# Performance work log

Measured on AMD Instinct MI355X. Metric: run time of the kernel, lower is better.

The kernel has to match this reference:

```python
import jax, jax.numpy as jnp
import numpy as np

B, N, C = 8, 8192, 256
H = 8            # num_heads
D = C // H       # head dim = 32
P = 64           # proj_size (Linformer rank)


def setup_inputs() -> dict:
    key = jax.random.key(0)
    ks = jax.random.split(key, 12)
    s = lambda fan_in: 1.0 / np.sqrt(fan_in)
    return {
        "x": jax.random.normal(ks[0], (B, N, C), jnp.float32),
        "Wqkvv": jax.random.normal(ks[1], (4 * C, C), jnp.float32) * s(C),
        "WE": jax.random.normal(ks[2], (P, N), jnp.float32) * s(N),
        "bE": jax.random.normal(ks[3], (P,), jnp.float32) * s(N),
        "WF": jax.random.normal(ks[4], (P, N), jnp.float32) * s(N),
        "bF": jax.random.normal(ks[5], (P,), jnp.float32) * s(N),
        "Wo1": jax.random.normal(ks[6], (C // 2, C), jnp.float32) * s(C),
        "bo1": jax.random.normal(ks[7], (C // 2,), jnp.float32) * s(C),
        "Wo2": jax.random.normal(ks[8], (C // 2, C), jnp.float32) * s(C),
        "bo2": jax.random.normal(ks[9], (C // 2,), jnp.float32) * s(C),
        "temp1": jnp.ones((H, 1, 1), jnp.float32),
        "temp2": jnp.ones((H, 1, 1), jnp.float32),
    }


def _l2norm(v, axis=-1, eps=1e-12):
    # matches torch F.normalize
    n = jnp.sqrt(jnp.sum(v * v, axis=axis, keepdims=True))
    return v / jnp.maximum(n, eps)


def reference(x, Wqkvv, WE, bE, WF, bF, Wo1, bo1, Wo2, bo2, temp1, temp2):
    b, n, c = x.shape
    # qkvv: [b,n,4c] -> [4,b,h,d,n]  (includes the .transpose(-2,-1) of each part)
    qkvv = jnp.einsum('bnc,fc->bnf', x, Wqkvv).reshape(b, n, 4, H, D)
    qkvv = qkvv.transpose(2, 0, 3, 4, 1)
    q, k, v_ca, v_sa = qkvv[0], qkvv[1], qkvv[2], qkvv[3]  # each [b,h,d,n]

    # Linformer-style low-rank projections along the token axis
    k_proj = jnp.einsum('bhdn,pn->bhdp', k, WE) + bE   # [b,h,d,p]
    v_proj = jnp.einsum('bhdn,pn->bhdp', v_sa, WF) + bF

    qn = _l2norm(q)
    kn = _l2norm(k)

    # --- channel attention branch (XCiT-style) ---
    attn_ca = jnp.einsum('bhdn,bhen->bhde', qn, kn) * temp1[None]  # [b,h,d,d]
    attn_ca = jax.nn.softmax(attn_ca, axis=-1)  # dropout: eval mode (identity)
    x_ca = jnp.einsum('bhde,bhen->bhdn', attn_ca, v_ca)
    x_ca = x_ca.transpose(0, 3, 1, 2).reshape(b, n, c)  # [b,n,c]

    # --- spatial attention branch (low-rank) ---
    attn_sa = jnp.einsum('bhdn,bhdp->bhnp', qn, k_proj) * temp2[None]  # [b,h,n,p]
    attn_sa = jax.nn.softmax(attn_sa, axis=-1)
    x_sa = jnp.einsum('bhnp,bhdp->bhnd', attn_sa, v_proj)  # [b,h,n,d]
    # faithful to original: permute(0,3,1,2).reshape(b,n,c)
    x_sa = x_sa.transpose(0, 3, 1, 2).reshape(b, n, c)

    x_sa = jnp.einsum('bnc,oc->bno', x_sa, Wo1) + bo1
    x_ca = jnp.einsum('bnc,oc->bno', x_ca, Wo2) + bo2
    return jnp.concatenate((x_sa, x_ca), axis=-1)
```

## Files before the change

kernel.cpp:

```cpp
#include <hip/hip_runtime.h>
#include <hip/hip_bf16.h>
#include <stdint.h>


typedef __attribute__((ext_vector_type(8))) __bf16 bf16x8;
typedef __attribute__((ext_vector_type(4))) __bf16 bf16x4;
typedef __attribute__((ext_vector_type(4))) float f32x4;

#define MFMA(a, b, c) __builtin_amdgcn_mfma_f32_16x16x32_bf16((a), (b), (c), 0, 0, 0)

__device__ __forceinline__ void gl2lds16(const __bf16* g, __bf16* l) {
  __builtin_amdgcn_global_load_lds(
      (const __attribute__((address_space(1))) void*)(const void*)g,
      (__attribute__((address_space(3))) void*)(void*)l, 16, 0, 0);
}

__device__ __forceinline__ int detect_f32(const unsigned int* __restrict__ xw) {
  int c = 0;
#pragma unroll
  for (int i = 0; i < 64; ++i) {
    const unsigned int u = xw[i];
    c += (((u >> 7) & 0xFF) >= 0xC0) ? 1 : 0;
    c += (((u >> 23) & 0xFF) >= 0xC0) ? 1 : 0;
  }
  return c > 8;
}

__global__ __launch_bounds__(256) void k_convert_x(const void* __restrict__ src,
                                                   __bf16* __restrict__ dst,
                                                   float* __restrict__ nsum) {
  if (blockIdx.x == 0) {
#pragma unroll
    for (int j = 0; j < 16; ++j) nsum[threadIdx.x + j * 256] = 0.f;
  }
  const int i = (blockIdx.x * 256 + threadIdx.x) * 8;
  if (detect_f32((const unsigned int*)src)) {
    const float* s = (const float*)src;
    bf16x8 v;
#pragma unroll
    for (int j = 0; j < 8; ++j) v[j] = (__bf16)s[i + j];
    *(bf16x8*)(dst + i) = v;
  } else {
    *(bf16x8*)(dst + i) = *(const bf16x8*)((const __bf16*)src + i);
  }
}

__global__ __launch_bounds__(256) void k_convert_w(
    const void* s0, const void* s1, const void* s2, const void* s3, const void* s4,
    const void* s5, const void* s6, const void* s7, const void* s8, const void* s9,
    const void* s10, __bf16* __restrict__ cw, const void* __restrict__ xsrc) {
  const int i = (blockIdx.x * 256 + threadIdx.x) * 8;
  if (i >= 1376656) return;
  const void* s;
  int base;
  if (i < 262144)        { s = s0;  base = 0; }
  else if (i < 786432)   { s = s1;  base = 262144; }
  else if (i < 786496)   { s = s2;  base = 786432; }
  else if (i < 1310784)  { s = s3;  base = 786496; }
  else if (i < 1310848)  { s = s4;  base = 1310784; }
  else if (i < 1343616)  { s = s5;  base = 1310848; }
  else if (i < 1343744)  { s = s6;  base = 1343616; }
  else if (i < 1376512)  { s = s7;  base = 1343744; }
  else if (i < 1376640)  { s = s8;  base = 1376512; }
  else if (i < 1376648)  { s = s9;  base = 1376640; }
  else                   { s = s10; base = 1376648; }
  const int li = i - base;
  if (detect_f32((const unsigned int*)xsrc)) {
    const float* sf = (const float*)s;
#pragma unroll
    for (int j = 0; j < 8; ++j) cw[i + j] = (__bf16)sf[li + j];
  } else {
    const __bf16* sb = (const __bf16*)s;
#pragma unroll
    for (int j = 0; j < 8; ++j) cw[i + j] = sb[li + j];
  }
}

__global__ __launch_bounds__(256) void k_qkvv(const __bf16* __restrict__ x,
                                              const __bf16* __restrict__ Wq,
                                              __bf16* __restrict__ qkvv,
                                              float* __restrict__ qsum,
                                              float* __restrict__ ksum) {
  __shared__ alignas(16) __bf16 As[128 * 32];
  __shared__ alignas(16) __bf16 Bs[128 * 32];
  const int t = threadIdx.x, lane = t & 63;
  const int wr = t >> 7, wc = (t >> 6) & 1;
  const int l15 = lane & 15, g = lane >> 4;
  const int f0 = blockIdx.y * 128;
  const int t0 = blockIdx.x * 128;
  f32x4 acc[4][4] = {};
  const int r = t >> 2;
  const int c8 = ((t & 3) ^ ((t >> 3) & 3)) * 8;
  const int cx = ((g ^ ((l15 >> 1) & 3)) * 8);
  for (int k0 = 0; k0 < 256; k0 += 32) {
#pragma unroll
    for (int i = 0; i < 2; ++i) {
      gl2lds16(Wq + (size_t)(f0 + i * 64 + r) * 256 + k0 + c8, As + i * 2048 + t * 8);
      gl2lds16(x + (size_t)(t0 + i * 64 + r) * 256 + k0 + c8, Bs + i * 2048 + t * 8);
    }
    __syncthreads();
    bf16x8 af[4], bfr[4];
#pragma unroll
    for (int i = 0; i < 4; ++i) {
      af[i] = *(const bf16x8*)(As + (wr * 64 + i * 16 + l15) * 32 + cx);
      bfr[i] = *(const bf16x8*)(Bs + (wc * 64 + i * 16 + l15) * 32 + cx);
    }
#pragma unroll
    for (int i = 0; i < 4; ++i)
#pragma unroll
      for (int j = 0; j < 4; ++j) acc[i][j] = MFMA(af[i], bfr[j], acc[i][j]);
    __syncthreads();
  }
  const int b = t0 >> 13;
#pragma unroll
  for (int i = 0; i < 4; ++i) {
#pragma unroll
    for (int j = 0; j < 4; ++j) {
      const int tok = t0 + wc * 64 + j * 16 + l15;
      const int n = tok & 8191;
#pragma unroll
      for (int rr = 0; rr < 4; ++rr) {
        const int f = f0 + wr * 64 + i * 16 + g * 4 + rr;
        qkvv[(size_t)(((f >> 8) * 8 + b) * 256 + (f & 255)) * 8192 + n] = (__bf16)acc[i][j][rr];
      }
    }
  }
  if (f0 < 512) {
    float* dst = (f0 >> 8) ? ksum : qsum;
#pragma unroll
    for (int i = 0; i < 4; ++i) {
#pragma unroll
      for (int rr = 0; rr < 4; ++rr) {
        float s = 0.f;
#pragma unroll
        for (int j = 0; j < 4; ++j) {
          const float v = acc[i][j][rr];
          s += v * v;
        }
#pragma unroll
        for (int off = 1; off < 16; off <<= 1) s += __shfl_xor(s, off, 16);
        if (l15 == 0) {
          const int f = f0 + wr * 64 + i * 16 + g * 4 + rr;
          atomicAdd(dst + b * 256 + (f & 255), s);
        }
      }
    }
  }
}

__global__ __launch_bounds__(256) void k_proj_part(const __bf16* __restrict__ qkvv,
                                                   const __bf16* __restrict__ WE,
                                                   const __bf16* __restrict__ WF,
                                                   float* __restrict__ pbuf) {
  __shared__ alignas(16) __bf16 As[128 * 32];
  __shared__ alignas(16) __bf16 Bs[64 * 32];
  const int t = threadIdx.x, lane = t & 63;
  const int wr = t >> 7, wc = (t >> 6) & 1;
  const int l15 = lane & 15, g = lane >> 4;
  const int kc = blockIdx.x, mt = blockIdx.y, pj = blockIdx.z;
  const __bf16* A = qkvv + (size_t)(pj ? 3 : 1) * 2048 * 8192;
  const __bf16* Bm = pj ? WF : WE;
  const int r0 = mt * 128;
  f32x4 acc[4][2] = {};
  const int r = t >> 2;
  const int c8 = ((t & 3) ^ ((t >> 3) & 3)) * 8;
  const int cx = ((g ^ ((l15 >> 1) & 3)) * 8);
  for (int k0 = kc * 512; k0 < kc * 512 + 512; k0 += 32) {
#pragma unroll
    for (int i = 0; i < 2; ++i)
      gl2lds16(A + (size_t)(r0 + i * 64 + r) * 8192 + k0 + c8, As + i * 2048 + t * 8);
    gl2lds16(Bm + (size_t)r * 8192 + k0 + c8, Bs + t * 8);
    __syncthreads();
    bf16x8 af[4], bfr[2];
#pragma unroll
    for (int i = 0; i < 4; ++i)
      af[i] = *(const bf16x8*)(As + (wr * 64 + i * 16 + l15) * 32 + cx);
#pragma unroll
    for (int j = 0; j < 2; ++j)
      bfr[j] = *(const bf16x8*)(Bs + (wc * 32 + j * 16 + l15) * 32 + cx);
#pragma unroll
    for (int i = 0; i < 4; ++i)
#pragma unroll
      for (int j = 0; j < 2; ++j) acc[i][j] = MFMA(af[i], bfr[j], acc[i][j]);
    __syncthreads();
  }
  float* dst = pbuf + (size_t)((pj * 16 + kc) * 2048 + r0) * 64;
#pragma unroll
  for (int i = 0; i < 4; ++i)
#pragma unroll
    for (int j = 0; j < 2; ++j)
#pragma unroll
      for (int rr = 0; rr < 4; ++rr)
        dst[(wr * 64 + i * 16 + g * 4 + rr) * 64 + wc * 32 + j * 16 + l15] = acc[i][j][rr];
}

__global__ __launch_bounds__(256) void k_proj_reduce(const float* __restrict__ pbuf,
                                                     const __bf16* __restrict__ bE,
                                                     const __bf16* __restrict__ bF,
                                                     const float* __restrict__ qsum,
                                                     const __bf16* __restrict__ t2,
                                                     __bf16* __restrict__ kprojT,
                                                     __bf16* __restrict__ vprojb) {
  const int idx = blockIdx.x * 256 + threadIdx.x;
  const int pj = idx >> 17, rp = idx & 131071, p = idx & 63;
  const int row = rp >> 6, bh = row >> 5, d = row & 31, h = bh & 7;
  float s = (float)((pj ? bF : bE)[p]);
  const float* src = pbuf + (size_t)pj * 16 * 131072 + rp;
#pragma unroll
  for (int k = 0; k < 16; ++k) s += src[(size_t)k * 131072];
  if (pj == 0) {
    const float qi = 1.0f / fmaxf(sqrtf(qsum[row]), 1e-12f);
    kprojT[bh * 2048 + p * 32 + d] = (__bf16)(s * qi * (float)t2[h]);
  } else {
    vprojb[bh * 2048 + d * 64 + p] = (__bf16)s;
  }
}

__global__ __launch_bounds__(256) void k_sca_part(const __bf16* __restrict__ qkvv,
                                                  float* __restrict__ spart) {
  const int bh = blockIdx.x, kc = blockIdx.y;
  const int t = threadIdx.x, lane = t & 63, w = t >> 6;
  const __bf16* qb = qkvv + (size_t)(bh * 32) * 8192;
  const __bf16* kb = qkvv + (size_t)(2048 + bh * 32) * 8192;
  f32x4 acc[2][2] = {};
  const int kbase = kc * 1024 + w * 256 + (lane >> 4) * 8;
#pragma unroll
  for (int ks = 0; ks < 256; ks += 32) {
    bf16x8 af[2], bfr[2];
#pragma unroll
    for (int i = 0; i < 2; ++i) {
      af[i] = *(const bf16x8*)(qb + (size_t)(i * 16 + (lane & 15)) * 8192 + kbase + ks);
      bfr[i] = *(const bf16x8*)(kb + (size_t)(i * 16 + (lane & 15)) * 8192 + kbase + ks);
    }
#pragma unroll
    for (int i = 0; i < 2; ++i)
#pragma unroll
      for (int j = 0; j < 2; ++j) acc[i][j] = MFMA(af[i], bfr[j], acc[i][j]);
  }
  float* dst = spart + (size_t)((bh * 8 + kc) * 4 + w) * 1024;
#pragma unroll
  for (int i = 0; i < 2; ++i)
#pragma unroll
    for (int j = 0; j < 2; ++j)
#pragma unroll
      for (int rr = 0; rr < 4; ++rr)
        dst[(i * 16 + (lane >> 4) * 4 + rr) * 32 + j * 16 + (lane & 15)] = acc[i][j][rr];
}

__global__ __launch_bounds__(256) void k_sca_softmax(const float* __restrict__ spart,
                                                     const float* __restrict__ qsum,
                                                     const float* __restrict__ ksum,
                                                     const __bf16* __restrict__ temp1,
                                                     __bf16* __restrict__ attnb) {
  const int bh = blockIdx.x;
  __shared__ float S[1024];
  const int t = threadIdx.x;
  const float tmp = (float)temp1[bh & 7];
  for (int idx = t; idx < 1024; idx += 256) {
    float s = 0.f;
    const float* src = spart + (size_t)bh * 32768 + idx;
#pragma unroll
    for (int k = 0; k < 32; ++k) s += src[k * 1024];
    const float qi = 1.0f / fmaxf(sqrtf(qsum[bh * 32 + (idx >> 5)]), 1e-12f);
    const float ki = 1.0f / fmaxf(sqrtf(ksum[bh * 32 + (idx & 31)]), 1e-12f);
    S[idx] = s * qi * ki * tmp;
  }
  __syncthreads();
  const int lane = t & 63, w = t >> 6;
#pragma unroll
  for (int rr = 0; rr < 4; ++rr) {
    const int row = rr * 8 + w * 2 + (lane >> 5);
    const int e = lane & 31;
    float v = S[row * 32 + e];
    float m = v;
#pragma unroll
    for (int off = 16; off; off >>= 1) m = fmaxf(m, __shfl_xor(m, off, 32));
    const float ex = __expf(v - m);
    float sm = ex;
#pragma unroll
    for (int off = 16; off; off >>= 1) sm += __shfl_xor(sm, off, 32);
    attnb[(size_t)bh * 1024 + row * 32 + e] = (__bf16)(ex / sm);
  }
}

__global__ __launch_bounds__(256) void k_casa(const __bf16* __restrict__ qkvv,
                                              const __bf16* __restrict__ attnb,
                                              const __bf16* __restrict__ kprojT,
                                              const __bf16* __restrict__ vprojb,
                                              __bf16* __restrict__ xca,
                                              __bf16* __restrict__ xsa) {
  __shared__ __bf16 P[4][16 * 72];
  const int t = threadIdx.x, lane = t & 63, w = t >> 6;
  const int l15 = lane & 15, g = lane >> 4;
  if (blockIdx.y < 64) {
    const int bh = blockIdx.y, b = bh >> 3, h = bh & 7;
    const __bf16* vb = qkvv + (size_t)(4096 + bh * 32) * 8192;
    bf16x8 aa[2];
#pragma unroll
    for (int mi = 0; mi < 2; ++mi)
      aa[mi] = *(const bf16x8*)(attnb + bh * 1024 + (mi * 16 + l15) * 32 + g * 8);
#pragma unroll
    for (int it = 0; it < 4; ++it) {
      const int n = blockIdx.x * 256 + it * 64 + w * 16 + l15;
      union { bf16x8 v; unsigned short u[8]; } bq;
#pragma unroll
      for (int j = 0; j < 8; ++j)
        bq.u[j] = *(const unsigned short*)(vb + (size_t)(g * 8 + j) * 8192 + n);
      f32x4 o[2] = {};
#pragma unroll
      for (int mi = 0; mi < 2; ++mi) o[mi] = MFMA(aa[mi], bq.v, o[mi]);
#pragma unroll
      for (int mi = 0; mi < 2; ++mi) {
        bf16x4 p4;
#pragma unroll
        for (int rr = 0; rr < 4; ++rr) p4[rr] = (__bf16)o[mi][rr];
        *(bf16x4*)(xca + (size_t)(b * 8192 + n) * 256 + h * 32 + mi * 16 + g * 4) = p4;
      }
    }
  } else {
    const int bh = blockIdx.y - 64;
    const __bf16* qb = qkvv + (size_t)(bh * 32) * 8192;
    bf16x8 ka[4], va[2][2];
#pragma unroll
    for (int tile = 0; tile < 4; ++tile)
      ka[tile] = *(const bf16x8*)(kprojT + bh * 2048 + (tile * 16 + l15) * 32 + g * 8);
#pragma unroll
    for (int mi = 0; mi < 2; ++mi)
#pragma unroll
      for (int kh = 0; kh < 2; ++kh)
        va[mi][kh] = *(const bf16x8*)(vprojb + bh * 2048 + (mi * 16 + l15) * 64 + kh * 32 + g * 8);
    __bf16* Pw = &P[w][0];
#pragma unroll
    for (int it = 0; it < 4; ++it) {
      const int n0 = blockIdx.x * 256 + it * 64 + w * 16;
      union { bf16x8 v; unsigned short u[8]; } bq;
#pragma unroll
      for (int j = 0; j < 8; ++j)
        bq.u[j] = *(const unsigned short*)(qb + (size_t)(g * 8 + j) * 8192 + n0 + l15);
      f32x4 st[4];
#pragma unroll
      for (int tile = 0; tile < 4; ++tile) {
        f32x4 z = {};
        st[tile] = MFMA(ka[tile], bq.v, z);
      }
      float m = st[0][0];
#pragma unroll
      for (int tile = 0; tile < 4; ++tile)
#pragma unroll
        for (int rr = 0; rr < 4; ++rr) m = fmaxf(m, st[tile][rr]);
      m = fmaxf(m, __shfl_xor(m, 16, 64));
      m = fmaxf(m, __shfl_xor(m, 32, 64));
      float sum = 0.f;
#pragma unroll
      for (int tile = 0; tile < 4; ++tile) {
        bf16x4 p4;
#pragma unroll
        for (int rr = 0; rr < 4; ++rr) {
          const float ex = __expf(st[tile][rr] - m);
          sum += ex;
          p4[rr] = (__bf16)ex;
        }
        *(bf16x4*)(Pw + l15 * 72 + tile * 16 + g * 4) = p4;
      }
      sum += __shfl_xor(sum, 16, 64);
      sum += __shfl_xor(sum, 32, 64);
      const float inv = 1.0f / sum;
      f32x4 o[2] = {};
#pragma unroll
      for (int kh = 0; kh < 2; ++kh) {
        const bf16x8 pf = *(const bf16x8*)(Pw + l15 * 72 + kh * 32 + g * 8);
#pragma unroll
        for (int mi = 0; mi < 2; ++mi) o[mi] = MFMA(va[mi][kh], pf, o[mi]);
      }
#pragma unroll
      for (int mi = 0; mi < 2; ++mi)
#pragma unroll
        for (int rr = 0; rr < 4; ++rr) {
          const int d = mi * 16 + g * 4 + rr;
          xsa[(size_t)(bh * 32 + d) * 8192 + n0 + l15] = (__bf16)(o[mi][rr] * inv);
        }
    }
  }
}

__global__ __launch_bounds__(256) void k_out(const __bf16* __restrict__ xsa,
                                             const __bf16* __restrict__ xca,
                                             const __bf16* __restrict__ Wo1,
                                             const __bf16* __restrict__ bo1,
                                             const __bf16* __restrict__ Wo2,
                                             const __bf16* __restrict__ bo2,
                                             void* __restrict__ outv,
                                             const void* __restrict__ xsrc) {
  __shared__ alignas(16) __bf16 As[128 * 32];
  __shared__ alignas(16) __bf16 Bs[128 * 32];
  const int t = threadIdx.x, lane = t & 63;
  const int wr = t >> 7, wc = (t >> 6) & 1;
  const int l15 = lane & 15, g = lane >> 4;
  const int nt = blockIdx.x, b = blockIdx.y, br = blockIdx.z;
  const int isf32 = detect_f32((const unsigned int*)xsrc);
  const __bf16* Wo = br ? Wo2 : Wo1;
  const __bf16* bo = br ? bo2 : bo1;
  f32x4 acc[4][4] = {};
  const int r = t >> 2;
  const int c8 = ((t & 3) ^ ((t >> 3) & 3)) * 8;
  const int cx = ((g ^ ((l15 >> 1) & 3)) * 8);
  for (int k0 = 0; k0 < 256; k0 += 32) {
#pragma unroll
    for (int i = 0; i < 2; ++i) {
      const int row = nt * 128 + i * 64 + r;
      const __bf16* ga;
      if (br == 0) {
        ga = xsa + (size_t)((b * 8 + ((row >> 5) & 7)) * 32 + (row >> 8)) * 8192 +
             (row & 31) * 256 + k0 + c8;
      } else {
        ga = xca + (size_t)(b * 8192 + row) * 256 + k0 + c8;
      }
      gl2lds16(ga, As + i * 2048 + t * 8);
      gl2lds16(Wo + (size_t)(i * 64 + r) * 256 + k0 + c8, Bs + i * 2048 + t * 8);
    }
    __syncthreads();
    bf16x8 af[4], bfr[4];
#pragma unroll
    for (int i = 0; i < 4; ++i) {
      af[i] = *(const bf16x8*)(As + (wr * 64 + i * 16 + l15) * 32 + cx);
      bfr[i] = *(const bf16x8*)(Bs + (wc * 64 + i * 16 + l15) * 32 + cx);
    }
#pragma unroll
    for (int i = 0; i < 4; ++i)
#pragma unroll
      for (int j = 0; j < 4; ++j) acc[i][j] = MFMA(af[i], bfr[j], acc[i][j]);
    __syncthreads();
  }
  float bias[4];
#pragma unroll
  for (int j = 0; j < 4; ++j) bias[j] = (float)bo[wc * 64 + j * 16 + l15];
#pragma unroll
  for (int i = 0; i < 4; ++i) {
#pragma unroll
    for (int j = 0; j < 4; ++j) {
      const int col = wc * 64 + j * 16 + l15;
#pragma unroll
      for (int rr = 0; rr < 4; ++rr) {
        const int row = nt * 128 + wr * 64 + i * 16 + g * 4 + rr;
        const float val = acc[i][j][rr] + bias[j];
        const size_t oi = (size_t)(b * 8192 + row) * 256 + br * 128 + col;
        if (isf32) ((float*)outv)[oi] = val;
        else ((__bf16*)outv)[oi] = (__bf16)val;
      }
    }
  }
}

extern "C" void kernel_launch(void* const* d_in, const int* in_sizes, int n_in,
                              void* d_out, int out_size, void* d_ws, size_t ws_size,
                              hipStream_t stream) {
  char* ws = (char*)d_ws;
  __bf16* qkvv   = (__bf16*)(ws);
  __bf16* cinx   = (__bf16*)(ws + 134217728ull);
  __bf16* xca    = (__bf16*)(ws + 134217728ull);
  float*  pbuf   = (float*)(ws + 167772160ull);
  float*  spart  = (float*)(ws + 184549376ull);
  __bf16* xsa    = (__bf16*)(ws + 167772160ull);
  __bf16* kprojT = (__bf16*)(ws + 201326592ull);
  __bf16* vprojb = (__bf16*)(ws + 201588736ull);
  float*  qsum   = (float*)(ws + 201850880ull);
  float*  ksum   = (float*)(ws + 201859072ull);
  __bf16* attnb  = (__bf16*)(ws + 201867264ull);
  __bf16* cw     = (__bf16*)(ws + 201998336ull);

  __bf16* cWq  = cw;
  __bf16* cWE  = cw + 262144;
  __bf16* cbE  = cw + 786432;
  __bf16* cWF  = cw + 786496;
  __bf16* cbF  = cw + 1310784;
  __bf16* cWo1 = cw + 1310848;
  __bf16* cbo1 = cw + 1343616;
  __bf16* cWo2 = cw + 1343744;
  __bf16* cbo2 = cw + 1376512;
  __bf16* ct1  = cw + 1376640;
  __bf16* ct2  = cw + 1376648;

  k_convert_x<<<8192, 256, 0, stream>>>(d_in[0], cinx, qsum);
  k_convert_w<<<673, 256, 0, stream>>>(d_in[1], d_in[2], d_in[3], d_in[4], d_in[5],
                                       d_in[6], d_in[7], d_in[8], d_in[9], d_in[10],
                                       d_in[11], cw, d_in[0]);
  k_qkvv<<<dim3(512, 8), 256, 0, stream>>>(cinx, cWq, qkvv, qsum, ksum);
  k_proj_part<<<dim3(16, 16, 2), 256, 0, stream>>>(qkvv, cWE, cWF, pbuf);
  k_proj_reduce<<<dim3(1024), 256, 0, stream>>>(pbuf, cbE, cbF, qsum, ct2, kprojT, vprojb);
  k_sca_part<<<dim3(64, 8), 256, 0, stream>>>(qkvv, spart);
  k_sca_softmax<<<dim3(64), 256, 0, stream>>>(spart, qsum, ksum, ct1, attnb);
  k_casa<<<dim3(32, 128), 256, 0, stream>>>(qkvv, attnb, kprojT, vprojb, xca, xsa);
  k_out<<<dim3(64, 8, 2), 256, 0, stream>>>(xsa, xca, cWo1, cbo1, cWo2, cbo2, d_out, d_in[0]);
}
```

Before: 330.0 us.

## Stage QKVV epilogue through LDS for coalesced stores; replace norm atomics with partial reduction

The QKVV GEMM epilogue now transposes each 16-row accumulator slice through a shared-memory tile so that every thread writes 16-byte contiguous runs along the token axis, replacing scattered 2-byte stores. The squared-norm sums for q and k are computed from the bf16-rounded values and written as per-block partials, and a new small kernel reduces them, so float atomics and the zeroing in the convert kernel are no longer needed. This adds LDS traffic, extra barriers and one more kernel launch. The norms now come from bf16-rounded values rather than the fp32 accumulators.

Result: faster. 311.5 us (-5.6%).

```diff
diff --git a/kernel.cpp b/kernel.cpp
--- a/kernel.cpp
+++ b/kernel.cpp
@@ -27,12 +27,7 @@
 }
 
 __global__ __launch_bounds__(256) void k_convert_x(const void* __restrict__ src,
-                                                   __bf16* __restrict__ dst,
-                                                   float* __restrict__ nsum) {
-  if (blockIdx.x == 0) {
-#pragma unroll
-    for (int j = 0; j < 16; ++j) nsum[threadIdx.x + j * 256] = 0.f;
-  }
+                                                   __bf16* __restrict__ dst) {
   const int i = (blockIdx.x * 256 + threadIdx.x) * 8;
   if (detect_f32((const unsigned int*)src)) {
     const float* s = (const float*)src;
@@ -79,10 +74,10 @@
 __global__ __launch_bounds__(256) void k_qkvv(const __bf16* __restrict__ x,
                                               const __bf16* __restrict__ Wq,
                                               __bf16* __restrict__ qkvv,
-                                              float* __restrict__ qsum,
-                                              float* __restrict__ ksum) {
+                                              float* __restrict__ npart) {
   __shared__ alignas(16) __bf16 As[128 * 32];
   __shared__ alignas(16) __bf16 Bs[128 * 32];
+  __shared__ alignas(16) __bf16 Cs[32 * 136];
   const int t = threadIdx.x, lane = t & 63;
   const int wr = t >> 7, wc = (t >> 6) & 1;
   const int l15 = lane & 15, g = lane >> 4;
@@ -112,40 +107,44 @@
     __syncthreads();
   }
   const int b = t0 >> 13;
-#pragma unroll
+  const int n0 = t0 & 8191;
   for (int i = 0; i < 4; ++i) {
-#pragma unroll
-    for (int j = 0; j < 4; ++j) {
-      const int tok = t0 + wc * 64 + j * 16 + l15;
-      const int n = tok & 8191;
-#pragma unroll
-      for (int rr = 0; rr < 4; ++rr) {
-        const int f = f0 + wr * 64 + i * 16 + g * 4 + rr;
-        qkvv[(size_t)(((f >> 8) * 8 + b) * 256 + (f & 255)) * 8192 + n] = (__bf16)acc[i][j][rr];
-      }
-    }
-  }
-  if (f0 < 512) {
-    float* dst = (f0 >> 8) ? ksum : qsum;
-#pragma unroll
-    for (int i = 0; i < 4; ++i) {
-#pragma unroll
-      for (int rr = 0; rr < 4; ++rr) {
+    if (i) __syncthreads();
+#pragma unroll
+    for (int j = 0; j < 4; ++j)
+#pragma unroll
+      for (int rr = 0; rr < 4; ++rr)
+        Cs[(wr * 16 + g * 4 + rr) * 136 + wc * 64 + j * 16 + l15] = (__bf16)acc[i][j][rr];
+    __syncthreads();
+#pragma unroll
+    for (int half = 0; half < 2; ++half) {
+      const int row_l = (t >> 4) + half * 16;
+      const int col8 = (t & 15) * 8;
+      const bf16x8 v = *(const bf16x8*)(Cs + row_l * 136 + col8);
+      const int f = f0 + (row_l >> 4) * 64 + i * 16 + (row_l & 15);
+      *(bf16x8*)(qkvv + (size_t)(((f >> 8) * 8 + b) * 256 + (f & 255)) * 8192 + n0 + col8) = v;
+      if (f0 < 512) {
         float s = 0.f;
 #pragma unroll
-        for (int j = 0; j < 4; ++j) {
-          const float v = acc[i][j][rr];
-          s += v * v;
-        }
+        for (int jj = 0; jj < 8; ++jj) { const float q = (float)v[jj]; s += q * q; }
 #pragma unroll
         for (int off = 1; off < 16; off <<= 1) s += __shfl_xor(s, off, 16);
-        if (l15 == 0) {
-          const int f = f0 + wr * 64 + i * 16 + g * 4 + rr;
-          atomicAdd(dst + b * 256 + (f & 255), s);
-        }
-      }
-    }
-  }
+        if ((t & 15) == 0) npart[(size_t)blockIdx.x * 512 + f] = s;
+      }
+    }
+  }
+}
+
+__global__ __launch_bounds__(256) void k_nred(const float* __restrict__ npart,
+                                              float* __restrict__ qsum,
+                                              float* __restrict__ ksum) {
+  const int which = blockIdx.x >> 3, b = blockIdx.x & 7;
+  const int c = threadIdx.x;
+  float s = 0.f;
+#pragma unroll 4
+  for (int j = 0; j < 64; ++j)
+    s += npart[(size_t)(b * 64 + j) * 512 + which * 256 + c];
+  (which ? ksum : qsum)[b * 256 + c] = s;
 }
 
 __global__ __launch_bounds__(256) void k_proj_part(const __bf16* __restrict__ qkvv,
@@ -459,6 +458,7 @@
   __bf16* cinx   = (__bf16*)(ws + 134217728ull);
   __bf16* xca    = (__bf16*)(ws + 134217728ull);
   float*  pbuf   = (float*)(ws + 167772160ull);
+  float*  npart  = (float*)(ws + 184549376ull);
   float*  spart  = (float*)(ws + 184549376ull);
   __bf16* xsa    = (__bf16*)(ws + 167772160ull);
   __bf16* kprojT = (__bf16*)(ws + 201326592ull);
@@ -480,11 +480,12 @@
   __bf16* ct1  = cw + 1376640;
   __bf16* ct2  = cw + 1376648;
 
-  k_convert_x<<<8192, 256, 0, stream>>>(d_in[0], cinx, qsum);
+  k_convert_x<<<8192, 256, 0, stream>>>(d_in[0], cinx);
   k_convert_w<<<673, 256, 0, stream>>>(d_in[1], d_in[2], d_in[3], d_in[4], d_in[5],
                                        d_in[6], d_in[7], d_in[8], d_in[9], d_in[10],
                                        d_in[11], cw, d_in[0]);
-  k_qkvv<<<dim3(512, 8), 256, 0, stream>>>(cinx, cWq, qkvv, qsum, ksum);
+  k_qkvv<<<dim3(512, 8), 256, 0, stream>>>(cinx, cWq, qkvv, npart);
+  k_nred<<<16, 256, 0, stream>>>(npart, qsum, ksum);
   k_proj_part<<<dim3(16, 16, 2), 256, 0, stream>>>(qkvv, cWE, cWF, pbuf);
   k_proj_reduce<<<dim3(1024), 256, 0, stream>>>(pbuf, cbE, cbF, qsum, ct2, kprojT, vprojb);
   k_sca_part<<<dim3(64, 8), 256, 0, stream>>>(qkvv, spart);
```
